# Kernel optimization log

Hardware: AMD Instinct MI355X
Metric: run time of the kernel (lower is better)

Reference implementation:

```python
import jax, jax.numpy as jnp
import numpy as np

HID = 5120       # hidden_size
H = 32           # num_heads (TP shard)
Q_RANK = 1536    # q_lora_rank
KV_RANK = 512    # kv_lora_rank
D_NOPE = 128     # qk_nope_head_dim
D_ROPE = 64      # qk_rope_head_dim
DV = 128         # v_head_dim
Q_HEAD = D_NOPE + D_ROPE
T = 2048
EPS = 1e-6
ROPE_BASE = 10000.0
SCALE = Q_HEAD ** -0.5
NEG = jnp.finfo(jnp.float32).min


def rmsnorm(x, w):
    return x * jax.lax.rsqrt(jnp.mean(x * x, axis=-1, keepdims=True) + EPS) * w


def rope(x, pos):
    # half-split (GPT-NeoX style) rotary; the torch module permutes weights in
    # _update_pe so that interleaved RoPE becomes exactly this half-split form.
    half = x.shape[-1] // 2
    inv = 1.0 / (ROPE_BASE ** (jnp.arange(half, dtype=jnp.float32) / half))
    ang = pos.astype(jnp.float32)[:, None] * inv          # [T, half]
    cos, sin = jnp.cos(ang), jnp.sin(ang)
    if x.ndim == 3:                                       # [T, H, D]
        cos, sin = cos[:, None, :], sin[:, None, :]
    x1, x2 = jnp.split(x, 2, axis=-1)
    return jnp.concatenate([x1 * cos - x2 * sin, x2 * cos + x1 * sin], axis=-1)


def setup_inputs() -> dict:
    key = jax.random.key(0)
    ks = jax.random.split(key, 10)
    s = 0.02
    return {
        'hidden_states': jax.random.normal(ks[0], (1, T, HID), jnp.float32),
        'position_ids': jnp.arange(T, dtype=jnp.int64),
        'w_q_a': jax.random.normal(ks[1], (Q_RANK, HID), jnp.float32) * s,
        'q_a_ln_w': jnp.ones((Q_RANK,), jnp.float32),
        'w_q_b': jax.random.normal(ks[2], (H * Q_HEAD, Q_RANK), jnp.float32) * s,
        'w_kv_a': jax.random.normal(ks[3], (KV_RANK + D_ROPE, HID), jnp.float32) * s,
        'kv_a_ln_w': jnp.ones((KV_RANK,), jnp.float32),
        'w_kc': jax.random.normal(ks[4], (H, D_NOPE, KV_RANK), jnp.float32) * s,
        'w_vc': jax.random.normal(ks[5], (H, KV_RANK, DV), jnp.float32) * s,
        'w_o': jax.random.normal(ks[6], (HID, H * DV), jnp.float32) * s,
    }


def reference(hidden_states, position_ids, w_q_a, q_a_ln_w, w_q_b, w_kv_a,
              kv_a_ln_w, w_kc, w_vc, w_o):
    h = hidden_states[0]                                   # [T, HID]
    t = h.shape[0]
    # q low-rank path: q_a_proj -> rmsnorm -> q_b_proj
    q = rmsnorm(h @ w_q_a.T, q_a_ln_w) @ w_q_b.T           # [T, H*Q_HEAD]
    q = q.reshape(t, H, Q_HEAD)
    q_nope, q_pe = q[..., :D_NOPE], q[..., D_NOPE:]
    # absorb kv_b (w_kc): project q into the latent kv space
    q_lat = jnp.einsum('thn,hnk->thk', q_nope, w_kc)       # [T, H, KV_RANK]
    # kv low-rank path (MQA-style shared latent)
    ckv_full = h @ w_kv_a.T                                # [T, KV_RANK+D_ROPE]
    ckv = rmsnorm(ckv_full[:, :KV_RANK], kv_a_ln_w)        # [T, KV_RANK]
    k_pe = rope(ckv_full[:, KV_RANK:], position_ids)       # [T, D_ROPE]
    q_pe = rope(q_pe, position_ids)                        # [T, H, D_ROPE]
    # full query/key in latent+pe space; key/value shared across heads
    qf = jnp.concatenate([q_lat, q_pe], axis=-1)           # [T, H, KV_RANK+D_ROPE]
    kf = jnp.concatenate([ckv, k_pe], axis=-1)             # [T, KV_RANK+D_ROPE]
    scores = jnp.einsum('thd,sd->hts', qf, kf) * SCALE     # [H, T, T]
    causal = jnp.tril(jnp.ones((t, t), dtype=bool))
    scores = jnp.where(causal[None], scores, NEG)
    p = jax.nn.softmax(scores, axis=-1)
    o = jnp.einsum('hts,sk->thk', p, ckv)                  # [T, H, KV_RANK]
    o = jnp.einsum('thk,hkv->thv', o, w_vc)                # [T, H, DV]
    out = o.reshape(t, H * DV) @ w_o.T                     # [T, HID]
    return out[None]
```

## Files before the change

kernel.cpp:

```cpp
#include <hip/hip_runtime.h>
#include <hip/hip_bf16.h>
#include <type_traits>

typedef __attribute__((ext_vector_type(8))) short short8;
typedef __attribute__((ext_vector_type(4))) float f32x4;
using bf16 = __hip_bfloat16;

#define T_SEQ 2048
#define NH 32
#define SCALE_F 0.07216878364870323f

__device__ inline unsigned short f2bf(float f) {
    unsigned u = __builtin_bit_cast(unsigned, f);
    return (unsigned short)((u + 0x7fffu + ((u >> 16) & 1u)) >> 16);
}

__device__ inline void gload_lds16(const void* g, void* l) {
    __builtin_amdgcn_global_load_lds(
        (const __attribute__((address_space(1))) unsigned*)g,
        (__attribute__((address_space(3))) unsigned*)l, 16, 0, 0);
}

__device__ inline void cvt8(const float* in, bf16* out, long v, float scale) {
    f32x4 a = *(const f32x4*)(in + v * 8), b = *(const f32x4*)(in + v * 8 + 4);
    short8 r;
    r[0] = (short)f2bf(a[0] * scale); r[1] = (short)f2bf(a[1] * scale);
    r[2] = (short)f2bf(a[2] * scale); r[3] = (short)f2bf(a[3] * scale);
    r[4] = (short)f2bf(b[0] * scale); r[5] = (short)f2bf(b[1] * scale);
    r[6] = (short)f2bf(b[2] * scale); r[7] = (short)f2bf(b[3] * scale);
    *(short8*)(out + v * 8) = r;
}

template <typename TC>
__global__ __launch_bounds__(512, 2) void gemm8p_kernel(
    const bf16* __restrict__ A, const bf16* __restrict__ B, TC* __restrict__ C,
    int K, int lda, int ldb, int ldc)
{
    extern __shared__ char Lds[];
    const int bm = blockIdx.y * 256, bn = blockIdx.x * 256;
    const int tid = threadIdx.x, lane = tid & 63, w = tid >> 6;
    const int l15 = lane & 15, lg = lane >> 4;
    const int wmr = (w >> 2) * 64;
    const int wnc = (w & 3) * 32;
    const int lrh = lane >> 3;
    const int scolb = ((lane & 7) * 16) ^ ((lane >> 3) << 4);
    const int rdswz = (l15 & 7) << 4;
    const bf16* Ab = A + (long)bm * lda;
    const bf16* Bb = B + (long)bn * ldb;
    const int nt = K >> 6;

    auto stage_half = [&](int tt, int isB, int h) {
        const int buf = tt & 1;
        const int k0 = (tt >= nt ? tt - nt : tt) << 6;
        const bf16* Base = isB ? Bb : Ab;
        const int ld = isB ? ldb : lda;
        const char* g = (const char*)Base
            + ((long)(h * 128 + w * 8 + lrh) * ld + k0) * 2 + scolb;
        char* l = Lds + buf * 65536 + isB * 32768 + h * 16384 + w * 1024;
        gload_lds16(g, l);
        gload_lds16(g + (long)128 * ld, l + 8192);
    };

    f32x4 acc[4][4][2] = {};
    stage_half(0, 0, 0); stage_half(0, 1, 1); stage_half(0, 0, 1);
    stage_half(0, 1, 0); stage_half(1, 0, 0); stage_half(1, 1, 1);
    asm volatile("s_waitcnt vmcnt(4)" ::: "memory");
    __builtin_amdgcn_s_barrier();

    for (int t = 0; t < nt; ++t) {
        const char* Bufp = Lds + (t & 1) * 65536;
        short8 aF[4][2], bF[2][2];
        #define ARD(mh, fi, ks) \
            (*(const short8*)(Bufp + (mh) * 16384 + (wmr + (fi) * 16 + l15) * 128 \
                              + (((ks) * 64 + lg * 16) ^ rdswz)))
        #define BRD(nh, nj, ks) \
            (*(const short8*)(Bufp + 32768 + (nh) * 16384 + (wnc + (nj) * 16 + l15) * 128 \
                              + (((ks) * 64 + lg * 16) ^ rdswz)))
        #define MFMA16(q) \
            __builtin_amdgcn_s_setprio(1); \
            _Pragma("unroll") for (int ks = 0; ks < 2; ++ks) \
            _Pragma("unroll") for (int fi = 0; fi < 4; ++fi) \
            _Pragma("unroll") for (int nj = 0; nj < 2; ++nj) \
                acc[q][fi][nj] = __builtin_amdgcn_mfma_f32_16x16x32_bf16( \
                    aF[fi][ks], bF[nj][ks], acc[q][fi][nj], 0, 0, 0); \
            __builtin_amdgcn_s_setprio(0);

        #pragma unroll
        for (int fi = 0; fi < 4; ++fi) { aF[fi][0] = ARD(0, fi, 0); aF[fi][1] = ARD(0, fi, 1); }
        #pragma unroll
        for (int nj = 0; nj < 2; ++nj) { bF[nj][0] = BRD(0, nj, 0); bF[nj][1] = BRD(0, nj, 1); }
        stage_half(t + 1, 0, 1);
        asm volatile("s_waitcnt lgkmcnt(8)" ::: "memory");
        __builtin_amdgcn_s_barrier();
        asm volatile("s_waitcnt lgkmcnt(0)" ::: "memory");
        __builtin_amdgcn_sched_barrier(0);
        MFMA16(0)
        __builtin_amdgcn_s_barrier();
        #pragma unroll
        for (int nj = 0; nj < 2; ++nj) { bF[nj][0] = BRD(1, nj, 0); bF[nj][1] = BRD(1, nj, 1); }
        stage_half(t + 1, 1, 0);
        __builtin_amdgcn_s_barrier();
        asm volatile("s_waitcnt lgkmcnt(0)" ::: "memory");
        __builtin_amdgcn_sched_barrier(0);
        MFMA16(1)
        __builtin_amdgcn_s_barrier();
        #pragma unroll
        for (int fi = 0; fi < 4; ++fi) { aF[fi][0] = ARD(1, fi, 0); aF[fi][1] = ARD(1, fi, 1); }
        stage_half(t + 2, 0, 0);
        __builtin_amdgcn_s_barrier();
        asm volatile("s_waitcnt lgkmcnt(0)" ::: "memory");
        __builtin_amdgcn_sched_barrier(0);
        MFMA16(2)
        __builtin_amdgcn_s_barrier();
        #pragma unroll
        for (int nj = 0; nj < 2; ++nj) { bF[nj][0] = BRD(0, nj, 0); bF[nj][1] = BRD(0, nj, 1); }
        stage_half(t + 2, 1, 1);
        __builtin_amdgcn_s_barrier();
        asm volatile("s_waitcnt lgkmcnt(0)" ::: "memory");
        __builtin_amdgcn_sched_barrier(0);
        MFMA16(3)
        asm volatile("s_waitcnt vmcnt(4)" ::: "memory");
        __builtin_amdgcn_s_barrier();
        #undef ARD
        #undef BRD
        #undef MFMA16
    }
    asm volatile("s_waitcnt vmcnt(0)" ::: "memory");
    const int QMH[4] = {0, 0, 1, 1}, QNH[4] = {0, 1, 1, 0};
    #pragma unroll
    for (int q = 0; q < 4; ++q)
        #pragma unroll
        for (int fi = 0; fi < 4; ++fi)
            #pragma unroll
            for (int nj = 0; nj < 2; ++nj)
                #pragma unroll
                for (int i = 0; i < 4; ++i) {
                    const int row = bm + QMH[q] * 128 + wmr + fi * 16 + lg * 4 + i;
                    const int col = bn + QNH[q] * 128 + wnc + nj * 16 + l15;
                    if constexpr (std::is_same<TC, float>::value)
                        C[(long)row * ldc + col] = acc[q][fi][nj][i];
                    else
                        ((unsigned short*)C)[(long)row * ldc + col] = f2bf(acc[q][fi][nj][i]);
                }
}

__global__ __launch_bounds__(256, 2) void gemmhw2_kernel(
    const bf16* __restrict__ A1, const bf16* __restrict__ B1, bf16* __restrict__ C1,
    int lda1, int ldb1, int ldc1, long aS1, long bS1, long cS1,
    const bf16* __restrict__ A2, const bf16* __restrict__ B2, bf16* __restrict__ C2,
    int lda2, int ldb2, int ldc2)
{
    const int b = blockIdx.x;
    const bf16* A; const bf16* B; bf16* C;
    int lda, ldb, ldc, bm, bn;
    if (b < 256) {
        const int z = b >> 3;
        A = A1 + (long)z * aS1; B = B1 + (long)z * bS1; C = C1 + (long)z * cS1;
        lda = lda1; ldb = ldb1; ldc = ldc1;
        bm = (b & 7) * 256; bn = 0;
    } else {
        const int bb = b - 256;
        A = A2; B = B2; C = C2;
        lda = lda2; ldb = ldb2; ldc = ldc2;
        bm = (bb >> 4) * 256; bn = (bb & 15) * 128;
    }
    const int K = 512;
    __shared__ __align__(16) short As[2][256 * 32];
    __shared__ __align__(16) short Bs[2][128 * 32];
    const int tid = threadIdx.x, lane = tid & 63, w = tid >> 6;
    const int l15 = lane & 15, lg = lane >> 4;
    const int wm = w >> 1, wn = w & 1;
    const int sx = (lane & 7) ^ (lane >> 3);
    const int lrh = lane >> 3;
    const int srp = sx >> 2;
    const int scol = (sx & 3) * 8;
    const bf16* Ab = A + (long)bm * lda;
    const bf16* Bb = B + (long)bn * ldb;

    auto stage = [&](int buf, int k0) {
        #pragma unroll
        for (int jj = 0; jj < 4; ++jj) {
            const int j = w * 4 + jj;
            const int srow = 2 * (j * 8 + lrh) + srp;
            gload_lds16(Ab + (long)srow * lda + k0 + scol, &As[buf][j * 512]);
        }
        #pragma unroll
        for (int jj = 0; jj < 2; ++jj) {
            const int j = w * 2 + jj;
            const int srow = 2 * (j * 8 + lrh) + srp;
            gload_lds16(Bb + (long)srow * ldb + k0 + scol, &Bs[buf][j * 512]);
        }
    };

    const int rslot = ((((l15 & 1) << 2) | lg) ^ (l15 >> 1)) << 4;
    const int lrow_lo = l15 >> 1;
    f32x4 acc[8][4] = {};
    const int nt = K >> 5;
    stage(0, 0);
    for (int t = 0; t < nt; ++t) {
        if (t + 1 < nt) {
            stage((t + 1) & 1, (t + 1) << 5);
            asm volatile("s_waitcnt vmcnt(6)" ::: "memory");
        } else {
            asm volatile("s_waitcnt vmcnt(0)" ::: "memory");
        }
        __builtin_amdgcn_s_barrier();
        __builtin_amdgcn_sched_barrier(0);
        const char* Ap = (const char*)&As[t & 1][0];
        const char* Bp = (const char*)&Bs[t & 1][0];
        short8 af[8], bf[4];
        #pragma unroll
        for (int fi = 0; fi < 8; ++fi)
            af[fi] = *(const short8*)(Ap + (wm * 64 + fi * 8 + lrow_lo) * 128 + rslot);
        #pragma unroll
        for (int nj = 0; nj < 4; ++nj)
            bf[nj] = *(const short8*)(Bp + (wn * 32 + nj * 8 + lrow_lo) * 128 + rslot);
        #pragma unroll
        for (int fi = 0; fi < 8; ++fi)
            #pragma unroll
            for (int nj = 0; nj < 4; ++nj)
                acc[fi][nj] = __builtin_amdgcn_mfma_f32_16x16x32_bf16(
                    af[fi], bf[nj], acc[fi][nj], 0, 0, 0);
        asm volatile("s_waitcnt lgkmcnt(0)" ::: "memory");
        __builtin_amdgcn_sched_barrier(0);
        __builtin_amdgcn_s_barrier();
        __builtin_amdgcn_sched_barrier(0);
    }
    #pragma unroll
    for (int fi = 0; fi < 8; ++fi)
        #pragma unroll
        for (int nj = 0; nj < 4; ++nj)
            #pragma unroll
            for (int i = 0; i < 4; ++i) {
                const int row = bm + wm * 128 + fi * 16 + lg * 4 + i;
                const int col = bn + wn * 64 + nj * 16 + l15;
                ((unsigned short*)C)[(long)row * ldc + col] = f2bf(acc[fi][nj][i]);
            }
}

#define GW_NXT 17
#define GW_EXX 8
template <typename TC>
__global__ __launch_bounds__(512, 4) void gemm8w_kernel(
    const bf16* __restrict__ A, const bf16* __restrict__ B, TC* __restrict__ C,
    int K, int lda, int ldb, int ldc,
    const float* __restrict__ cv1in, bf16* __restrict__ cv1out, long n1v, float s1,
    const float* __restrict__ cv2in, bf16* __restrict__ cv2out, long n2v)
{
    const int tid = threadIdx.x;
    if (blockIdx.x >= GW_NXT) {
        const int cb = (blockIdx.x - GW_NXT) * gridDim.y + blockIdx.y;
        const long stride = (long)GW_EXX * gridDim.y * 512;
        for (long v = (long)cb * 512 + tid; v < n1v + n2v; v += stride) {
            if (v < n1v) cvt8(cv1in, cv1out, v, s1);
            else         cvt8(cv2in, cv2out, v - n1v, 1.f);
        }
        return;
    }
    const int bm = blockIdx.y * 128, bn = blockIdx.x * 128;
    __shared__ __align__(16) short As[2][128 * 64];
    __shared__ __align__(16) short Bs[2][128 * 64];
    const int lane = tid & 63, w = tid >> 6;
    const int l15 = lane & 15, lg = lane >> 4;
    const int wm = w >> 1, wn = w & 1;
    const int c0 = w * 2, c1 = w * 2 + 1;
    const int srow0 = c0 * 8 + (lane >> 3), srow1 = c1 * 8 + (lane >> 3);
    const int scol = ((lane & 7) * 16) ^ ((lane >> 3) << 4);
    const bf16* Ab = A + (long)bm * lda;
    const bf16* Bb = B + (long)bn * ldb;

    auto stage = [&](int buf, int k0) {
        const char* ag = (const char*)(Ab + k0);
        const char* bg = (const char*)(Bb + k0);
        gload_lds16(ag + (long)srow0 * (lda * 2) + scol, &As[buf][c0 * 512]);
        gload_lds16(ag + (long)srow1 * (lda * 2) + scol, &As[buf][c1 * 512]);
        gload_lds16(bg + (long)srow0 * (ldb * 2) + scol, &Bs[buf][c0 * 512]);
        gload_lds16(bg + (long)srow1 * (ldb * 2) + scol, &Bs[buf][c1 * 512]);
    };

    const int swz = (l15 & 7) << 4;
    f32x4 acc[2][4] = {};
    const int nt = K >> 6;
    stage(0, 0);
    for (int t = 0; t < nt; ++t) {
        if (t + 1 < nt) {
            stage((t + 1) & 1, (t + 1) << 6);
            asm volatile("s_waitcnt vmcnt(4)" ::: "memory");
        } else {
            asm volatile("s_waitcnt vmcnt(0)" ::: "memory");
        }
        __builtin_amdgcn_s_barrier();
        __builtin_amdgcn_sched_barrier(0);
        const char* Ap = (const char*)&As[t & 1][0];
        const char* Bp = (const char*)&Bs[t & 1][0];
        short8 af[2][2], bfv[4][2];
        #pragma unroll
        for (int fi = 0; fi < 2; ++fi)
            #pragma unroll
            for (int ks = 0; ks < 2; ++ks)
                af[fi][ks] = *(const short8*)(Ap + (wm * 32 + fi * 16 + l15) * 128
                                              + ((ks * 64 + lg * 16) ^ swz));
        #pragma unroll
        for (int nj = 0; nj < 4; ++nj)
            #pragma unroll
            for (int ks = 0; ks < 2; ++ks)
                bfv[nj][ks] = *(const short8*)(Bp + (wn * 64 + nj * 16 + l15) * 128
                                               + ((ks * 64 + lg * 16) ^ swz));
        #pragma unroll
        for (int ks = 0; ks < 2; ++ks)
            #pragma unroll
            for (int fi = 0; fi < 2; ++fi)
                #pragma unroll
                for (int nj = 0; nj < 4; ++nj)
                    acc[fi][nj] = __builtin_amdgcn_mfma_f32_16x16x32_bf16(
                        af[fi][ks], bfv[nj][ks], acc[fi][nj], 0, 0, 0);
        asm volatile("s_waitcnt lgkmcnt(0)" ::: "memory");
        __builtin_amdgcn_sched_barrier(0);
        __builtin_amdgcn_s_barrier();
        __builtin_amdgcn_sched_barrier(0);
    }
    #pragma unroll
    for (int fi = 0; fi < 2; ++fi)
        #pragma unroll
        for (int nj = 0; nj < 4; ++nj)
            #pragma unroll
            for (int i = 0; i < 4; ++i) {
                const int row = bm + wm * 32 + fi * 16 + lg * 4 + i;
                const int col = bn + wn * 64 + nj * 16 + l15;
                if constexpr (std::is_same<TC, float>::value)
                    C[(long)row * ldc + col] = acc[fi][nj][i];
                else
                    ((unsigned short*)C)[(long)row * ldc + col] = f2bf(acc[fi][nj][i]);
            }
}

__global__ __launch_bounds__(256) void cvtall_kernel(
    const float* __restrict__ hid, bf16* __restrict__ hb,
    const float* __restrict__ wqa, const float* __restrict__ wkva,
    bf16* __restrict__ wqckv,
    const float* __restrict__ wvc, bf16* __restrict__ wvct)
{
    if (blockIdx.x >= 2048) {
        const int idx = blockIdx.x - 2048;
        const int h = idx >> 6, d0 = ((idx >> 4) & 3) * 32, k0 = (idx & 15) * 32;
        __shared__ float t[32][33];
        const int r = threadIdx.x >> 5, c = threadIdx.x & 31;
        const float* ip = wvc + ((long)h * 512 + k0) * 128 + d0;
        #pragma unroll
        for (int it = 0; it < 4; ++it)
            t[r + 8 * it][c] = ip[(long)(r + 8 * it) * 128 + c];
        __syncthreads();
        bf16* op = wvct + ((long)h * 128 + d0) * 512 + k0;
        #pragma unroll
        for (int it = 0; it < 4; ++it)
            op[(long)(r + 8 * it) * 512 + c] = __float2bfloat16(t[c][r + 8 * it]);
        return;
    }
    const long N0 = (long)T_SEQ * 5120 / 8;
    const long N1 = N0 + (long)1536 * 5120 / 8;
    const long N2 = N1 + (long)576 * 5120 / 8;
    const long N3 = N2 + (long)64 * 5120 / 8;
    const long stride = (long)2048 * 256;
    for (long v = (long)blockIdx.x * 256 + threadIdx.x; v < N3; v += stride) {
        if (v < N0) cvt8(hid, hb, v, 1.f);
        else if (v < N1) cvt8(wqa, wqckv, v - N0, 1.f);
        else if (v < N2) cvt8(wkva, wqckv + (long)1536 * 5120, v - N1, 1.f);
        else {
            short8 z = {};
            *(short8*)(wqckv + (long)2112 * 5120 + (v - N2) * 8) = z;
        }
    }
}

__global__ __launch_bounds__(256) void rmsnorm2_kernel(
    bf16* __restrict__ x1, const float* __restrict__ w1, int C1,
    bf16* __restrict__ x2, const float* __restrict__ w2, int C2, int ld)
{
    bf16* row;
    const float* w;
    int C;
    if (blockIdx.x < 2048) { row = x1 + (long)blockIdx.x * ld; w = w1; C = C1; }
    else { row = x2 + (long)(blockIdx.x - 2048) * ld; w = w2; C = C2; }
    float ss = 0.f;
    for (int i = threadIdx.x; i < C; i += 256) {
        float v = __bfloat162float(row[i]);
        ss += v * v;
    }
    #pragma unroll
    for (int m = 1; m < 64; m <<= 1) ss += __shfl_xor(ss, m, 64);
    __shared__ float red[4];
    if ((threadIdx.x & 63) == 0) red[threadIdx.x >> 6] = ss;
    __syncthreads();
    ss = red[0] + red[1] + red[2] + red[3];
    float scale = rsqrtf(ss / (float)C + 1e-6f);
    for (int i = threadIdx.x; i < C; i += 256) {
        float v = __bfloat162float(row[i]);
        row[i] = __float2bfloat16(v * scale * w[i]);
    }
}

__global__ __launch_bounds__(256) void ropeq_kernel(bf16* __restrict__ q)
{
    const int t = blockIdx.x;
    #pragma unroll
    for (int it = 0; it < 4; ++it) {
        const int pair = threadIdx.x + 256 * it;
        const int h = pair >> 5, i = pair & 31;
        bf16* base = q + ((long)t * NH + h) * 192;
        float x1 = __bfloat162float(base[128 + i]);
        float x2 = __bfloat162float(base[160 + i]);
        float inv = powf(10000.f, -(float)i / 32.f);
        float ang = (float)t * inv, s, c;
        sincosf(ang, &s, &c);
        base[128 + i] = __float2bfloat16(x1 * c - x2 * s);
        base[160 + i] = __float2bfloat16(x2 * c + x1 * s);
    }
}

__global__ __launch_bounds__(1024) void ropek_kernel(
    const bf16* __restrict__ ckv, bf16* __restrict__ kf, int ld)
{
    const int t = blockIdx.x;
    const int h = threadIdx.x >> 5, i = threadIdx.x & 31;
    float x1 = __bfloat162float(ckv[(long)t * ld + 512 + i]);
    float x2 = __bfloat162float(ckv[(long)t * ld + 544 + i]);
    float inv = powf(10000.f, -(float)i / 32.f);
    float ang = (float)t * inv, s, c;
    sincosf(ang, &s, &c);
    bf16* kb = kf + ((long)h * T_SEQ + t) * 192;
    kb[128 + i] = __float2bfloat16(x1 * c - x2 * s);
    kb[160 + i] = __float2bfloat16(x2 * c + x1 * s);
}

__global__ __launch_bounds__(256, 2) void attn_kernel(
    const bf16* __restrict__ Q,
    const bf16* __restrict__ Kf,
    const bf16* __restrict__ Vt,
    bf16* __restrict__ O,
    const float* __restrict__ WOin, bf16* __restrict__ WOout)
{
    if (blockIdx.x >= 512) {
        const long base = ((long)blockIdx.x - 512) * 2048 + threadIdx.x;
        #pragma unroll
        for (int it = 0; it < 8; ++it)
            cvt8(WOin, WOout, base + (long)it * 256, 1.f);
        return;
    }
    const int lin = blockIdx.x;
    const int h = (lin & 7) + 8 * ((lin >> 3) & 3);
    const int qraw = lin >> 5;
    const int qblk = (qraw < 8) ? (2 * qraw) : (31 - 2 * qraw);
    const int q0 = qblk * 128;
    const int tid = threadIdx.x, lane = tid & 63, w = tid >> 6;
    const int l15 = lane & 15, lg = lane >> 4;
    const int qw = q0 + w * 32;
    __shared__ __align__(16) short Ks[64 * 192];
    __shared__ __align__(16) short Vs[128 * 64];

    int ksoff[6];
    #pragma unroll
    for (int j = 0; j < 6; ++j) {
        int o = (w * 6 + j) * 1024 + lane * 16;
        int row = o / 384, col = o % 384;
        ksoff[j] = row * 384 + (col ^ ((row & 7) << 4));
    }
    const int vrow8 = lane >> 3;
    const int vscol = ((lane & 7) * 16) ^ (vrow8 << 4);

    short8 qf[2][6];
    #pragma unroll
    for (int qi = 0; qi < 2; ++qi) {
        const bf16* qp = Q + (long)(qw + qi * 16 + l15) * (NH * 192) + (long)h * 192;
        #pragma unroll
        for (int c = 0; c < 6; ++c) qf[qi][c] = *(const short8*)(qp + c * 32 + lg * 8);
    }

    f32x4 oacc[2][8] = {};
    float mst[2] = {-INFINITY, -INFINITY};
    float lst[2] = {0.f, 0.f};

    const char* kbase0 = (const char*)Kf + (long)h * T_SEQ * 384;
    const char* vbase0 = (const char*)Vt + (long)h * 128 * (T_SEQ * 2);
    const int swz = (l15 & 7) << 4;

    for (int s0 = 0; s0 < q0 + 128; s0 += 64) {
        {
            const char* kb = kbase0 + (long)s0 * 384;
            #pragma unroll
            for (int j = 0; j < 6; ++j)
                gload_lds16(kb + ksoff[j], (char*)Ks + (w * 6 + j) * 1024);
            const char* vb = vbase0 + (long)s0 * 2 + vscol;
            #pragma unroll
            for (int j = 0; j < 4; ++j) {
                const int c = w * 4 + j;
                gload_lds16(vb + (long)(c * 8 + vrow8) * (T_SEQ * 2),
                            (char*)Vs + c * 1024);
            }
        }
        __syncthreads();
        if (s0 <= qw + 31) {
            f32x4 st[2][4] = {};
            __builtin_amdgcn_s_setprio(1);
            #pragma unroll
            for (int cb = 0; cb < 4; ++cb) {
                const int krow = cb * 16 + l15;
                #pragma unroll
                for (int c = 0; c < 6; ++c) {
                    short8 kfr = *(const short8*)((const char*)Ks + krow * 384
                                                  + ((c * 64 + lg * 16) ^ swz));
                    st[0][cb] = __builtin_amdgcn_mfma_f32_16x16x32_bf16(kfr, qf[0][c], st[0][cb], 0, 0, 0);
                    st[1][cb] = __builtin_amdgcn_mfma_f32_16x16x32_bf16(kfr, qf[1][c], st[1][cb], 0, 0, 0);
                }
            }
            __builtin_amdgcn_s_setprio(0);
            float pmaxv[2];
            #pragma unroll
            for (int qi = 0; qi < 2; ++qi) {
                const int qg = qw + qi * 16 + l15;
                float pmax = -INFINITY;
                #pragma unroll
                for (int cb = 0; cb < 4; ++cb)
                    #pragma unroll
                    for (int i = 0; i < 4; ++i) {
                        const int kv = s0 + cb * 16 + lg * 4 + i;
                        float v = (kv <= qg) ? st[qi][cb][i] : -INFINITY;
                        st[qi][cb][i] = v;
                        pmax = fmaxf(pmax, v);
                    }
                pmax = fmaxf(pmax, __shfl_xor(pmax, 16, 64));
                pmax = fmaxf(pmax, __shfl_xor(pmax, 32, 64));
                pmaxv[qi] = pmax;
            }
            const bool full = !__all((pmaxv[0] - mst[0] <= 8.f) &&
                                     (pmaxv[1] - mst[1] <= 8.f));
            short8 pb[2][2];
            #pragma unroll
            for (int qi = 0; qi < 2; ++qi) {
                float mm;
                if (full) {
                    const float newm = fmaxf(mst[qi], pmaxv[qi]);
                    mm = (newm == -INFINITY) ? 0.f : newm;
                    const float alpha = __expf(mst[qi] - mm);
                    lst[qi] *= alpha;
                    mst[qi] = newm;
                    #pragma unroll
                    for (int mb = 0; mb < 8; ++mb) oacc[qi][mb] *= alpha;
                } else {
                    mm = mst[qi];
                }
                float ps = 0.f;
                #pragma unroll
                for (int cb = 0; cb < 4; ++cb)
                    #pragma unroll
                    for (int i = 0; i < 4; ++i) {
                        const float e = __expf(st[qi][cb][i] - mm);
                        st[qi][cb][i] = e; ps += e;
                    }
                ps += __shfl_xor(ps, 16, 64);
                ps += __shfl_xor(ps, 32, 64);
                lst[qi] += ps;
                #pragma unroll
                for (int hh = 0; hh < 2; ++hh) {
                    unsigned pk[4];
                    #pragma unroll
                    for (int i = 0; i < 4; ++i)
                        pk[i] = (unsigned)f2bf(st[qi][2 * hh][i])
                              | ((unsigned)f2bf(st[qi][2 * hh + 1][i]) << 16);
                    #pragma unroll
                    for (int j = 0; j < 8; ++j) {
                        const int src = l15 + (((2 * lg + (j >> 2)) & 3) << 4);
                        const unsigned u = (unsigned)__shfl((int)pk[j & 3], src, 64);
                        pb[qi][hh][j] = (short)((lg >> 1) ? (u >> 16) : (u & 0xffffu));
                    }
                }
            }
            __builtin_amdgcn_s_setprio(1);
            #pragma unroll
            for (int mb = 0; mb < 8; ++mb) {
                const int vrow = mb * 16 + l15;
                #pragma unroll
                for (int hh = 0; hh < 2; ++hh) {
                    short8 vfr = *(const short8*)((const char*)Vs + vrow * 128
                                                  + ((hh * 64 + lg * 16) ^ swz));
                    oacc[0][mb] = __builtin_amdgcn_mfma_f32_16x16x32_bf16(vfr, pb[0][hh], oacc[0][mb], 0, 0, 0);
                    oacc[1][mb] = __builtin_amdgcn_mfma_f32_16x16x32_bf16(vfr, pb[1][hh], oacc[1][mb], 0, 0, 0);
                }
            }
            __builtin_amdgcn_s_setprio(0);
        }
        __syncthreads();
    }
    #pragma unroll
    for (int qi = 0; qi < 2; ++qi) {
        const float inv = 1.f / lst[qi];
        const int qg = qw + qi * 16 + l15;
        #pragma unroll
        for (int mb = 0; mb < 8; ++mb)
            #pragma unroll
            for (int i = 0; i < 4; ++i) {
                const int dv = mb * 16 + lg * 4 + i;
                O[(long)qg * (NH * 128) + h * 128 + dv] = __float2bfloat16(oacc[qi][mb][i] * inv);
            }
    }
}

extern "C" void kernel_launch(void* const* d_in, const int* in_sizes, int n_in,
                              void* d_out, int out_size, void* d_ws, size_t ws_size,
                              hipStream_t stream)
{
    const float* hidden    = (const float*)d_in[0];
    const float* w_q_a     = (const float*)d_in[2];
    const float* q_a_ln_w  = (const float*)d_in[3];
    const float* w_q_b     = (const float*)d_in[4];
    const float* w_kv_a    = (const float*)d_in[5];
    const float* kv_a_ln_w = (const float*)d_in[6];
    const float* w_kc      = (const float*)d_in[7];
    const float* w_vc      = (const float*)d_in[8];
    const float* w_o       = (const float*)d_in[9];
    float* out = (float*)d_out;

    bf16* qckv  = (bf16*)d_ws;
    bf16* qbuf  = qckv  + (long)T_SEQ * 2176;
    bf16* kf    = qbuf  + (long)T_SEQ * 6144;
    bf16* vt    = kf    + (long)NH * T_SEQ * 192;
    bf16* ov    = vt    + (long)NH * 128 * T_SEQ;
    bf16* hb    = ov    + (long)T_SEQ * 4096;
    bf16* wqckv = hb    + (long)T_SEQ * 5120;
    bf16* wqb   = wqckv + (long)2176 * 5120;
    bf16* wkc   = wqb   + (long)6144 * 1536;
    bf16* wvct  = wkc   + (long)NH * 128 * 512;
    bf16* wo    = hb;
    bf16* ckv   = qckv + 1536;

    cvtall_kernel<<<dim3(4096), 256, 0, stream>>>(
        hidden, hb, w_q_a, w_kv_a, wqckv, w_vc, wvct);

    gemm8w_kernel<bf16><<<dim3(GW_NXT + GW_EXX, 16, 1), 512, 0, stream>>>(
        hb, wqckv, qckv, 5120, 5120, 5120, 2176,
        w_q_b, wqb, (long)6144 * 1536 / 8, SCALE_F,
        w_kc, wkc, (long)NH * 128 * 512 / 8);
    rmsnorm2_kernel<<<dim3(4096), 256, 0, stream>>>(
        qckv, q_a_ln_w, 1536, ckv, kv_a_ln_w, 512, 2176);
    gemm8p_kernel<bf16><<<dim3(24, 8), 512, 131072, stream>>>(
        qckv, wqb, qbuf, 1536, 2176, 1536, 6144);
    ropeq_kernel<<<dim3(T_SEQ), 256, 0, stream>>>(qbuf);
    ropek_kernel<<<dim3(T_SEQ), 1024, 0, stream>>>(ckv, kf, 2176);
    gemmhw2_kernel<<<dim3(512), 256, 0, stream>>>(
        ckv, wkc, kf, 2176, 512, 192,
        0, (long)128 * 512, (long)T_SEQ * 192,
        wvct, ckv, vt, 512, 2176, 2048);
    attn_kernel<<<dim3(1792), 256, 0, stream>>>(qbuf, kf, vt, ov, w_o, wo);
    gemm8p_kernel<float><<<dim3(20, 8), 512, 131072, stream>>>(
        ov, wo, out, 4096, 4096, 4096, 5120);
}
```

Before: 420.8 us.

## Fuse query RoPE into attention prologue and key RoPE into latent GEMM launch

Removes the two standalone RoPE kernels. Query rotary embedding is now applied in registers inside the attention kernel right after the Q fragments are loaded, and key RoPE runs in 32 extra blocks appended to the gemmhw2 launch. This saves two kernel launches and the global read and write of the rope parts of q. In exchange the attention kernel recomputes sincos per block, and the extra gemmhw2 blocks write k_pe into kf concurrently with the GEMM blocks that fill the nope columns of the same rows.

```diff
diff --git a/kernel.cpp b/kernel.cpp
--- a/kernel.cpp
+++ b/kernel.cpp
@@ -13,6 +13,11 @@
 __device__ inline unsigned short f2bf(float f) {
     unsigned u = __builtin_bit_cast(unsigned, f);
     return (unsigned short)((u + 0x7fffu + ((u >> 16) & 1u)) >> 16);
+}
+
+__device__ inline float bfs2f(short s) {
+    unsigned u = ((unsigned)(unsigned short)s) << 16;
+    return __builtin_bit_cast(float, u);
 }
 
 __device__ inline void gload_lds16(const void* g, void* l) {
@@ -151,6 +156,28 @@
     int lda2, int ldb2, int ldc2)
 {
     const int b = blockIdx.x;
+    if (b >= 512) {
+        const int b2 = b - 512;
+        const int i = threadIdx.x & 31;
+        const int h0 = (threadIdx.x >> 5) * 4;
+        const float inv = powf(10000.f, -(float)i / 32.f);
+        for (int tt = 0; tt < 64; ++tt) {
+            const int t = b2 * 64 + tt;
+            const float x1 = __bfloat162float(A1[(long)t * lda1 + 512 + i]);
+            const float x2 = __bfloat162float(A1[(long)t * lda1 + 544 + i]);
+            float s, c;
+            sincosf((float)t * inv, &s, &c);
+            const bf16 o1 = __float2bfloat16(x1 * c - x2 * s);
+            const bf16 o2 = __float2bfloat16(x2 * c + x1 * s);
+            #pragma unroll
+            for (int hh = 0; hh < 4; ++hh) {
+                bf16* kb = C1 + ((long)(h0 + hh) * T_SEQ + t) * 192;
+                kb[128 + i] = o1;
+                kb[160 + i] = o2;
+            }
+        }
+        return;
+    }
     const bf16* A; const bf16* B; bf16* C;
     int lda, ldb, ldc, bm, bn;
     if (b < 256) {
@@ -399,39 +426,6 @@
     }
 }
 
-__global__ __launch_bounds__(256) void ropeq_kernel(bf16* __restrict__ q)
-{
-    const int t = blockIdx.x;
-    #pragma unroll
-    for (int it = 0; it < 4; ++it) {
-        const int pair = threadIdx.x + 256 * it;
-        const int h = pair >> 5, i = pair & 31;
-        bf16* base = q + ((long)t * NH + h) * 192;
-        float x1 = __bfloat162float(base[128 + i]);
-        float x2 = __bfloat162float(base[160 + i]);
-        float inv = powf(10000.f, -(float)i / 32.f);
-        float ang = (float)t * inv, s, c;
-        sincosf(ang, &s, &c);
-        base[128 + i] = __float2bfloat16(x1 * c - x2 * s);
-        base[160 + i] = __float2bfloat16(x2 * c + x1 * s);
-    }
-}
-
-__global__ __launch_bounds__(1024) void ropek_kernel(
-    const bf16* __restrict__ ckv, bf16* __restrict__ kf, int ld)
-{
-    const int t = blockIdx.x;
-    const int h = threadIdx.x >> 5, i = threadIdx.x & 31;
-    float x1 = __bfloat162float(ckv[(long)t * ld + 512 + i]);
-    float x2 = __bfloat162float(ckv[(long)t * ld + 544 + i]);
-    float inv = powf(10000.f, -(float)i / 32.f);
-    float ang = (float)t * inv, s, c;
-    sincosf(ang, &s, &c);
-    bf16* kb = kf + ((long)h * T_SEQ + t) * 192;
-    kb[128 + i] = __float2bfloat16(x1 * c - x2 * s);
-    kb[160 + i] = __float2bfloat16(x2 * c + x1 * s);
-}
-
 __global__ __launch_bounds__(256, 2) void attn_kernel(
     const bf16* __restrict__ Q,
     const bf16* __restrict__ Kf,
@@ -473,6 +467,20 @@
         const bf16* qp = Q + (long)(qw + qi * 16 + l15) * (NH * 192) + (long)h * 192;
         #pragma unroll
         for (int c = 0; c < 6; ++c) qf[qi][c] = *(const short8*)(qp + c * 32 + lg * 8);
+    }
+    #pragma unroll
+    for (int e = 0; e < 8; ++e) {
+        const float inv = powf(10000.f, -(float)(lg * 8 + e) / 32.f);
+        #pragma unroll
+        for (int qi = 0; qi < 2; ++qi) {
+            const float tpos = (float)(qw + qi * 16 + l15);
+            float s, c;
+            sincosf(tpos * inv, &s, &c);
+            const float x1 = bfs2f(qf[qi][4][e]);
+            const float x2 = bfs2f(qf[qi][5][e]);
+            qf[qi][4][e] = (short)f2bf(x1 * c - x2 * s);
+            qf[qi][5][e] = (short)f2bf(x2 * c + x1 * s);
+        }
     }
 
     f32x4 oacc[2][8] = {};
@@ -643,9 +651,7 @@
         qckv, q_a_ln_w, 1536, ckv, kv_a_ln_w, 512, 2176);
     gemm8p_kernel<bf16><<<dim3(24, 8), 512, 131072, stream>>>(
         qckv, wqb, qbuf, 1536, 2176, 1536, 6144);
-    ropeq_kernel<<<dim3(T_SEQ), 256, 0, stream>>>(qbuf);
-    ropek_kernel<<<dim3(T_SEQ), 1024, 0, stream>>>(ckv, kf, 2176);
-    gemmhw2_kernel<<<dim3(512), 256, 0, stream>>>(
+    gemmhw2_kernel<<<dim3(544), 256, 0, stream>>>(
         ckv, wkc, kf, 2176, 512, 192,
         0, (long)128 * 512, (long)T_SEQ * 192,
         wvct, ckv, vt, 512, 2176, 2048);
```

New measurement: 432.5 us. 2.8% more time.
